# Optimization experiments

Hardware: AMD Instinct MI355X
Metric: run time of the kernel (lower is better)

The kernel has to match this reference:

```python
import jax, jax.numpy as jnp
import numpy as np

B, C, H, W = 64, 3, 512, 512


def setup_inputs() -> dict:
    key = jax.random.key(0)
    k1, k2, k3 = jax.random.split(key, 3)
    img = jax.random.normal(k1, (B, C, H, W), dtype=jnp.float32)
    rot = jax.random.normal(k2, (B,), dtype=jnp.float32)          # radians
    trans = jax.random.normal(k3, (B, 2), dtype=jnp.float32) * 0.1
    scale = jnp.ones((B,), dtype=jnp.float32)
    return {"img": img, "rot": rot, "trans": trans, "scale": scale}


def reference(img, rot, trans, scale):
    # Batched equivalent of the per-image loop:
    #   theta = [[cos/s, -sin/s, tx], [sin/s, cos/s, ty]]  (2x3 per image)
    #   grid  = F.affine_grid(theta, img.size())           (align_corners=False)
    #   out   = F.grid_sample(img, grid)                    (bilinear, zeros pad)
    b_, c_, h_, w_ = img.shape
    cs = jnp.cos(rot) / scale
    sn = jnp.sin(rot) / scale

    # Base normalized grid (align_corners=False): x_i = (2i+1)/W - 1
    xs = (2.0 * jnp.arange(w_, dtype=img.dtype) + 1.0) / w_ - 1.0
    ys = (2.0 * jnp.arange(h_, dtype=img.dtype) + 1.0) / h_ - 1.0
    gy, gx = jnp.meshgrid(ys, xs, indexing="ij")  # [H, W]

    # Apply affine: [gx', gy'] = theta @ [gx, gy, 1]
    gx_t = cs[:, None, None] * gx + (-sn)[:, None, None] * gy + trans[:, 0, None, None]
    gy_t = sn[:, None, None] * gx + cs[:, None, None] * gy + trans[:, 1, None, None]

    # Unnormalize (align_corners=False): ix = ((g+1)*W - 1)/2
    ix = ((gx_t + 1.0) * w_ - 1.0) * 0.5
    iy = ((gy_t + 1.0) * h_ - 1.0) * 0.5

    x0 = jnp.floor(ix)
    y0 = jnp.floor(iy)
    wx1 = ix - x0  # frac weights
    wy1 = iy - y0
    x0i = x0.astype(jnp.int32)
    y0i = y0.astype(jnp.int32)

    bidx = jnp.arange(b_)[:, None, None]  # [B,1,1]

    def corner(yi, xi, w):
        valid = (xi >= 0) & (xi < w_) & (yi >= 0) & (yi < h_)
        yc = jnp.clip(yi, 0, h_ - 1)
        xc = jnp.clip(xi, 0, w_ - 1)
        v = img[bidx, :, yc, xc]  # [B,H,W,C] gather
        return v * (w * valid)[..., None]

    out = (
        corner(y0i, x0i, (1.0 - wy1) * (1.0 - wx1))
        + corner(y0i, x0i + 1, (1.0 - wy1) * wx1)
        + corner(y0i + 1, x0i, wy1 * (1.0 - wx1))
        + corner(y0i + 1, x0i + 1, wy1 * wx1)
    )
    return jnp.transpose(out, (0, 3, 1, 2))  # [B,C,H,W]
```

## Files before the change

### kernel.cpp

```cpp
#include <hip/hip_runtime.h>
#include <stdint.h>

#define BB 64
#define CC 3
#define HH 512
#define WW 512
#define TILE 32
#define MAXBH 48
#define MAXBW 52
#define PLST 60

typedef float f32x4 __attribute__((ext_vector_type(4)));

__device__ __forceinline__ void pix2in(float x, float y,
                                       float cs, float sn, float tx, float ty,
                                       float& ix, float& iy)
{
    float gx = (2.0f * x + 1.0f) * (1.0f / (float)WW) - 1.0f;
    float gy = (2.0f * y + 1.0f) * (1.0f / (float)HH) - 1.0f;
    float gxt = cs * gx - sn * gy + tx;
    float gyt = sn * gx + cs * gy + ty;
    ix = ((gxt + 1.0f) * (float)WW - 1.0f) * 0.5f;
    iy = ((gyt + 1.0f) * (float)HH - 1.0f) * 0.5f;
}

__global__ __launch_bounds__(256) void warp_setup(
    const float* __restrict__ rot, const float* __restrict__ trans,
    const float* __restrict__ scale, float* __restrict__ ws)
{
    const int i = blockIdx.x * 256 + threadIdx.x;
    const int b = i >> 8, t = i & 255;
    const float r = rot[b];
    const float inv_s = 1.0f / scale[b];
    const float cs = cosf(r) * inv_s;
    const float sn = sinf(r) * inv_s;
    const float tx = trans[2 * b], ty = trans[2 * b + 1];
    if (t == 0)
        reinterpret_cast<float4*>(ws)[b] = make_float4(cs, sn, tx, ty);

    const int oy0 = (t >> 4) * TILE;
    const int ox0 = (t & 15) * TILE;
    float ixa, iya, ixb, iyb, ixc, iyc, ixd, iyd;
    pix2in((float)ox0,              (float)oy0,              cs, sn, tx, ty, ixa, iya);
    pix2in((float)(ox0 + TILE - 1), (float)oy0,              cs, sn, tx, ty, ixb, iyb);
    pix2in((float)ox0,              (float)(oy0 + TILE - 1), cs, sn, tx, ty, ixc, iyc);
    pix2in((float)(ox0 + TILE - 1), (float)(oy0 + TILE - 1), cs, sn, tx, ty, ixd, iyd);
    const float minix = fminf(fminf(ixa, ixb), fminf(ixc, ixd));
    const float maxix = fmaxf(fmaxf(ixa, ixb), fmaxf(ixc, ixd));
    const float miniy = fminf(fminf(iya, iyb), fminf(iyc, iyd));
    const float maxiy = fmaxf(fmaxf(iya, iyb), fmaxf(iyc, iyd));
    const int bx0 = (int)floorf(minix) - 1;
    const int bx1 = (int)floorf(maxix) + 2;
    const int by0 = (int)floorf(miniy) - 1;
    const int by1 = (int)floorf(maxiy) + 2;
    int bx0c = bx0 & ~3;
    const int bw = bx1 - bx0c + 1;
    const int bh = by1 - by0 + 1;

    const uint32_t fit      = (bw <= MAXBW && bh <= MAXBH) ? 1u : 0u;
    const uint32_t interior = (bx0c >= 0 && bx1 < WW && by0 >= 0 && by1 < HH) ? 1u : 0u;
    const int bx0s = min(max(bx0c, -2048), 2047);
    const int by0s = min(max(by0,  -2048), 2047);
    const int bhs  = min(bh, 63);
    const uint32_t desc = ((uint32_t)bx0s & 0xFFFu)
                        | (((uint32_t)by0s & 0xFFFu) << 12)
                        | ((uint32_t)bhs << 24)
                        | (fit << 30) | (interior << 31);
    reinterpret_cast<uint32_t*>(ws)[256 + i] = desc;
}

template <bool INTERIOR>
__device__ __forceinline__ void compute_store(
    const float* __restrict__ pl, float* __restrict__ outb,
    int tid, int ox0, int oy0, int bx0c, int by0,
    float cs, float sn, float tpx, float tpy, long plane)
{
    const int ry = tid >> 5;
    const int xp = tid & 31;
    const int ox = ox0 + xp;

    float ix0, iy0;
    pix2in((float)ox, (float)(oy0 + ry), cs, sn, tpx, tpy, ix0, iy0);

    #pragma unroll
    for (int h = 0; h < 2; ++h) {
        const float ix = fmaf((float)(16 * h), -sn, ix0);
        const float iy = fmaf((float)(16 * h),  cs, iy0);
        const float x0f = floorf(ix), y0f = floorf(iy);
        const float wx1 = ix - x0f,  wy1 = iy - y0f;
        const float wx0 = 1.0f - wx1, wy0 = 1.0f - wy1;
        const int x0 = (int)x0f, y0 = (int)y0f;

        float w00 = wy0 * wx0, w01 = wy0 * wx1, w10 = wy1 * wx0, w11 = wy1 * wx1;
        if (!INTERIOR) {
            const int x1 = x0 + 1, y1 = y0 + 1;
            const float vx0 = (x0 >= 0 && x0 < WW) ? 1.0f : 0.0f;
            const float vx1 = (x1 >= 0 && x1 < WW) ? 1.0f : 0.0f;
            const float vy0 = (y0 >= 0 && y0 < HH) ? 1.0f : 0.0f;
            const float vy1 = (y1 >= 0 && y1 < HH) ? 1.0f : 0.0f;
            w00 *= vy0 * vx0; w01 *= vy0 * vx1; w10 *= vy1 * vx0; w11 *= vy1 * vx1;
        }

        const int idx = (y0 - by0) * PLST + (x0 - bx0c);
        const float* pb = pl + idx;
        const int oy = oy0 + ry + 16 * h;
        const long ob = (long)oy * WW + ox;
        #pragma unroll
        for (int c = 0; c < CC; ++c) {
            const float* pc = pb + c * (MAXBH * PLST);
            const float v = w00 * pc[0] + w01 * pc[1]
                          + w10 * pc[PLST] + w11 * pc[PLST + 1];
            __builtin_nontemporal_store(v, outb + c * plane + ob);
        }
    }
}

__global__ __launch_bounds__(512) void warp_tiled(
    const float* __restrict__ img, const float* __restrict__ ws,
    float* __restrict__ out)
{
    __shared__ __align__(16) float pl[CC][MAXBH][PLST];

    const int g   = blockIdx.x;
    const int swz = (g & 7) * ((BB * 256) / 8) + (g >> 3);
    const int b   = swz >> 8;
    const int t   = swz & 255;
    const int oy0 = (t >> 4) * TILE;
    const int ox0 = (t & 15) * TILE;

    const float4 p = reinterpret_cast<const float4*>(ws)[b];
    const float cs = p.x, sn = p.y, tpx = p.z, tpy = p.w;
    const uint32_t desc = reinterpret_cast<const uint32_t*>(ws)[256 + swz];
    const int  bx0c     = ((int)(desc << 20)) >> 20;
    const int  by0      = ((int)(desc << 8))  >> 20;
    const int  bh       = (desc >> 24) & 63;
    const bool fit      = (desc >> 30) & 1;
    const bool interior = (desc >> 31) & 1;

    const long plane = (long)HH * WW;
    const float* imb = img + (long)b * CC * plane;
    float* outb      = out + (long)b * CC * plane;
    const int tid = threadIdx.x;

    if (fit) {
        const int q  = tid >> 4;
        const int ql = tid & 15;
        if (ql < 13) {
            const int xb = ql * 4;
            if (interior && (bx0c + 51 < WW)) {
                for (int r = q; r < bh; r += 32) {
                    const float* pr = imb + (long)(by0 + r) * WW + (bx0c + xb);
                    const f32x4 a = *reinterpret_cast<const f32x4*>(pr);
                    const f32x4 bv = *reinterpret_cast<const f32x4*>(pr + plane);
                    const f32x4 cv = *reinterpret_cast<const f32x4*>(pr + 2 * plane);
                    *reinterpret_cast<f32x4*>(&pl[0][r][xb]) = a;
                    *reinterpret_cast<f32x4*>(&pl[1][r][xb]) = bv;
                    *reinterpret_cast<f32x4*>(&pl[2][r][xb]) = cv;
                }
            } else {
                for (int r = q; r < bh; r += 32) {
                    const int grow = by0 + r;
                    const bool rowok = (grow >= 0) && (grow < HH);
                    const float* pr = imb + (long)grow * WW;
                    f32x4 a = {0.f, 0.f, 0.f, 0.f}, bv = a, cv = a;
                    #pragma unroll
                    for (int k = 0; k < 4; ++k) {
                        const int gcol = bx0c + xb + k;
                        if (rowok && gcol >= 0 && gcol < WW) {
                            a[k]  = pr[gcol];
                            bv[k] = pr[(long)gcol + plane];
                            cv[k] = pr[(long)gcol + 2 * plane];
                        }
                    }
                    *reinterpret_cast<f32x4*>(&pl[0][r][xb]) = a;
                    *reinterpret_cast<f32x4*>(&pl[1][r][xb]) = bv;
                    *reinterpret_cast<f32x4*>(&pl[2][r][xb]) = cv;
                }
            }
        }
        __syncthreads();

        if (interior)
            compute_store<true >(&pl[0][0][0], outb, tid, ox0, oy0, bx0c, by0, cs, sn, tpx, tpy, plane);
        else
            compute_store<false>(&pl[0][0][0], outb, tid, ox0, oy0, bx0c, by0, cs, sn, tpx, tpy, plane);
    } else {
        #pragma unroll
        for (int k = 0; k < 2; ++k) {
            const int pidx = tid + k * 512;
            const int py = pidx >> 5;
            const int px = pidx & 31;
            const int ox = ox0 + px, oy = oy0 + py;

            float ix, iy;
            pix2in((float)ox, (float)oy, cs, sn, tpx, tpy, ix, iy);
            const float x0f = floorf(ix), y0f = floorf(iy);
            const float wx1 = ix - x0f,  wy1 = iy - y0f;
            const int x0 = (int)x0f, y0 = (int)y0f;
            const int x1 = x0 + 1,  y1 = y0 + 1;

            const float vx0 = (x0 >= 0 && x0 < WW) ? 1.0f : 0.0f;
            const float vx1 = (x1 >= 0 && x1 < WW) ? 1.0f : 0.0f;
            const float vy0 = (y0 >= 0 && y0 < HH) ? 1.0f : 0.0f;
            const float vy1 = (y1 >= 0 && y1 < HH) ? 1.0f : 0.0f;

            const int x0c = min(max(x0, 0), WW - 1);
            const int x1c = min(max(x1, 0), WW - 1);
            const int y0c = min(max(y0, 0), HH - 1);
            const int y1c = min(max(y1, 0), HH - 1);

            const float w00 = (1.0f - wy1) * (1.0f - wx1) * vy0 * vx0;
            const float w01 = (1.0f - wy1) * wx1          * vy0 * vx1;
            const float w10 = wy1          * (1.0f - wx1) * vy1 * vx0;
            const float w11 = wy1          * wx1          * vy1 * vx1;

            const int o00 = y0c * WW + x0c, o01 = y0c * WW + x1c;
            const int o10 = y1c * WW + x0c, o11 = y1c * WW + x1c;
            const int ob = oy * WW + ox;
            #pragma unroll
            for (int c = 0; c < CC; ++c) {
                const float* pc = imb + (long)c * plane;
                const float v = w00 * pc[o00] + w01 * pc[o01]
                              + w10 * pc[o10] + w11 * pc[o11];
                __builtin_nontemporal_store(v, &outb[(long)c * plane + ob]);
            }
        }
    }
}

extern "C" void kernel_launch(void* const* d_in, const int* in_sizes, int n_in,
                              void* d_out, int out_size, void* d_ws, size_t ws_size,
                              hipStream_t stream) {
    const float* img   = (const float*)d_in[0];
    const float* rot   = (const float*)d_in[1];
    const float* trans = (const float*)d_in[2];
    const float* scale = (const float*)d_in[3];
    float* out = (float*)d_out;
    float* ws  = (float*)d_ws;

    warp_setup<<<dim3(BB), 256, 0, stream>>>(rot, trans, scale, ws);
    warp_tiled<<<dim3(BB * 256), 512, 0, stream>>>(img, ws, out);
}
```

Before: 68.25 us.

## Load interior tiles with direct global-to-LDS DMA and XOR-swizzled shared layout

Replaces the register-staged vector loads of interior source patches with global_load_lds 16-byte direct-to-LDS transfers. It also changes the shared-memory layout to a 64-float row stride with an XOR swizzle of 4-float chunks by row, which the DMA lane mapping requires and which is meant to limit bank conflicts on bilinear reads. The DMA path loads 64 columns per row instead of 52 and needs more index arithmetic per tap in the compute phase. It also relies on the builtin's per-wave LDS base semantics being correct.

```diff
diff --git a/kernel.cpp b/kernel.cpp
--- a/kernel.cpp
+++ b/kernel.cpp
@@ -8,9 +8,18 @@
 #define TILE 32
 #define MAXBH 48
 #define MAXBW 52
-#define PLST 60
+#define RSD 64
+#define CHSTD (MAXBH * RSD)
 
 typedef float f32x4 __attribute__((ext_vector_type(4)));
+
+__device__ __forceinline__ void gload_lds16(const float* src, float* lds)
+{
+    __builtin_amdgcn_global_load_lds(
+        (const __attribute__((address_space(1))) unsigned int*)src,
+        (__attribute__((address_space(3))) unsigned int*)lds,
+        16, 0, 0);
+}
 
 __device__ __forceinline__ void pix2in(float x, float y,
                                        float cs, float sn, float tx, float ty,
@@ -101,15 +110,23 @@
             w00 *= vy0 * vx0; w01 *= vy0 * vx1; w10 *= vy1 * vx0; w11 *= vy1 * vx1;
         }
 
-        const int idx = (y0 - by0) * PLST + (x0 - bx0c);
-        const float* pb = pl + idx;
+        const int ly0 = y0 - by0;
+        const int ly1 = ly0 + 1;
+        const int lx0 = x0 - bx0c;
+        const int lx1 = lx0 + 1;
+        const int k0 = ly0 & 15, k1 = ly1 & 15;
+        const int s00 = (ly0 << 6) + ((((lx0 >> 2) ^ k0) << 2) | (lx0 & 3));
+        const int s01 = (ly0 << 6) + ((((lx1 >> 2) ^ k0) << 2) | (lx1 & 3));
+        const int s10 = (ly1 << 6) + ((((lx0 >> 2) ^ k1) << 2) | (lx0 & 3));
+        const int s11 = (ly1 << 6) + ((((lx1 >> 2) ^ k1) << 2) | (lx1 & 3));
+
         const int oy = oy0 + ry + 16 * h;
         const long ob = (long)oy * WW + ox;
         #pragma unroll
         for (int c = 0; c < CC; ++c) {
-            const float* pc = pb + c * (MAXBH * PLST);
-            const float v = w00 * pc[0] + w01 * pc[1]
-                          + w10 * pc[PLST] + w11 * pc[PLST + 1];
+            const float* pc = pl + c * CHSTD;
+            const float v = w00 * pc[s00] + w01 * pc[s01]
+                          + w10 * pc[s10] + w11 * pc[s11];
             __builtin_nontemporal_store(v, outb + c * plane + ob);
         }
     }
@@ -119,7 +136,7 @@
     const float* __restrict__ img, const float* __restrict__ ws,
     float* __restrict__ out)
 {
-    __shared__ __align__(16) float pl[CC][MAXBH][PLST];
+    __shared__ __align__(16) float pl[CC][MAXBH][RSD];
 
     const int g   = blockIdx.x;
     const int swz = (g & 7) * ((BB * 256) / 8) + (g >> 3);
@@ -143,21 +160,27 @@
     const int tid = threadIdx.x;
 
     if (fit) {
-        const int q  = tid >> 4;
-        const int ql = tid & 15;
-        if (ql < 13) {
-            const int xb = ql * 4;
-            if (interior && (bx0c + 51 < WW)) {
-                for (int r = q; r < bh; r += 32) {
-                    const float* pr = imb + (long)(by0 + r) * WW + (bx0c + xb);
-                    const f32x4 a = *reinterpret_cast<const f32x4*>(pr);
-                    const f32x4 bv = *reinterpret_cast<const f32x4*>(pr + plane);
-                    const f32x4 cv = *reinterpret_cast<const f32x4*>(pr + 2 * plane);
-                    *reinterpret_cast<f32x4*>(&pl[0][r][xb]) = a;
-                    *reinterpret_cast<f32x4*>(&pl[1][r][xb]) = bv;
-                    *reinterpret_cast<f32x4*>(&pl[2][r][xb]) = cv;
+        const bool dma = interior && (bx0c + 63 < WW);
+        if (dma) {
+            const int wid   = tid >> 6;
+            const int rin   = (tid & 63) >> 4;
+            const int chunk = tid & 15;
+            const int rbmax = (bh + 3) >> 2;
+            for (int ch = 0; ch < CC; ++ch) {
+                const float* pc = imb + (long)ch * plane;
+                for (int rb = wid; rb < rbmax; rb += 8) {
+                    const int r    = rb * 4 + rin;
+                    const int grow = min(by0 + r, HH - 1);
+                    const int sch  = chunk ^ (r & 15);
+                    const float* src = pc + (long)grow * WW + bx0c + sch * 4;
+                    gload_lds16(src, &pl[ch][rb * 4][0]);
                 }
-            } else {
+            }
+        } else {
+            const int q  = tid >> 4;
+            const int ql = tid & 15;
+            if (ql < 13) {
+                const int xb = ql * 4;
                 for (int r = q; r < bh; r += 32) {
                     const int grow = by0 + r;
                     const bool rowok = (grow >= 0) && (grow < HH);
@@ -172,9 +195,10 @@
                             cv[k] = pr[(long)gcol + 2 * plane];
                         }
                     }
-                    *reinterpret_cast<f32x4*>(&pl[0][r][xb]) = a;
-                    *reinterpret_cast<f32x4*>(&pl[1][r][xb]) = bv;
-                    *reinterpret_cast<f32x4*>(&pl[2][r][xb]) = cv;
+                    const int slot4 = (ql ^ (r & 15)) << 2;
+                    *reinterpret_cast<f32x4*>(&pl[0][r][slot4]) = a;
+                    *reinterpret_cast<f32x4*>(&pl[1][r][slot4]) = bv;
+                    *reinterpret_cast<f32x4*>(&pl[2][r][slot4]) = cv;
                 }
             }
         }
```

Result: no change. 67.96 us (-0.4%).
